# Kernel optimization log

Measured on AMD Instinct MI355X. Metric: run time of the kernel, lower is better.

The kernel has to match this reference:

```python
import jax, jax.numpy as jnp
import numpy as np

LAMB = 1.0
EPS = 1e-16


def setup_inputs() -> dict:
    key = jax.random.key(0)
    kx, km = jax.random.split(key)
    N, D, K = 262144, 128, 64
    x = jax.random.normal(kx, (N, D), dtype=jnp.float32)
    m = jax.random.normal(km, (K, D), dtype=jnp.float32)
    m = m / jnp.linalg.norm(m, axis=1, keepdims=True)  # unit-norm rows like __init__
    return {"x": x, "m": m}


def _entropy(p):
    # replicate torch.where clamping
    p = jnp.where(p <= 0, EPS, p)
    p = jnp.where(p >= 1, 1.0 - EPS, p)
    return -jnp.sum(p * jnp.log(p), axis=-1)


def _p(x, m):
    d2 = (jnp.sum(x * x, axis=-1, keepdims=True)
          - 2.0 * x @ m.T
          + jnp.sum(m * m, axis=-1))  # [N, K]
    return jax.nn.softmax(-d2, axis=-1)


def reference(x, m):
    p = _p(x, m)                      # [N, K]
    intra = jnp.mean(_entropy(p))     # scalar
    mu = jnp.mean(m, axis=0)          # [D]
    p_inter = _p(mu[None, :], m)[0]   # [K]
    inter = _entropy(p_inter)
    total = intra - LAMB * inter
    return (total, intra, inter)
```

## Files before the change

kernel.cpp:

```cpp
#include <hip/hip_runtime.h>
#include <hip/hip_bf16.h>

#define D 128
#define K 64

typedef __attribute__((ext_vector_type(8))) short short8;
typedef __attribute__((ext_vector_type(4))) float f32x4;

__device__ inline short f2bf(float f) {
  union { float f; unsigned u; } v; v.f = f;
  unsigned u = v.u;
  return (short)((u + 0x7fffu + ((u >> 16) & 1u)) >> 16);
}

__global__ void prep_kernel(const float* __restrict__ m, float* ws) {
  int tid = threadIdx.x;
  if (tid < 16) ws[tid] = 0.0f;
  if (tid < K) {
    const float* mr = m + tid * D;
    float s = 0.f;
    for (int d = 0; d < D; ++d) s += mr[d] * mr[d];
    ws[16 + tid] = s;
  }
  short* mb = (short*)(ws + 128);
  for (int i = tid; i < K * D; i += blockDim.x) mb[i] = f2bf(2.0f * m[i]);
}

__launch_bounds__(256)
__global__ void main_kernel(const float* __restrict__ x, float* ws, int nTiles, int totalWaves) {
  const float* mnorm = ws + 16;
  const short* mb = (const short*)(ws + 128);
  const int lane = threadIdx.x & 63;
  const int lid  = lane & 15;
  const int quad = lane >> 4;

  short8 bfr[4][4];
  float mn[4];
#pragma unroll
  for (int jt = 0; jt < 4; ++jt) {
    mn[jt] = mnorm[jt * 16 + lid];
#pragma unroll
    for (int kk = 0; kk < 4; ++kk)
      bfr[jt][kk] = *(const short8*)(mb + (jt * 16 + lid) * D + kk * 32 + quad * 8);
  }

  const int wave = blockIdx.x * (blockDim.x >> 6) + (threadIdx.x >> 6);
  float hacc = 0.f;

  for (int t = wave; t < nTiles; t += totalWaves) {
    const float* xb = x + (size_t)(t * 16 + lid) * D + quad * 8;
    short8 a[4];
#pragma unroll
    for (int kk = 0; kk < 4; ++kk) {
      f32x4 v0 = *(const f32x4*)(xb + kk * 32);
      f32x4 v1 = *(const f32x4*)(xb + kk * 32 + 4);
      short8 av;
      av[0] = f2bf(v0[0]); av[1] = f2bf(v0[1]); av[2] = f2bf(v0[2]); av[3] = f2bf(v0[3]);
      av[4] = f2bf(v1[0]); av[5] = f2bf(v1[1]); av[6] = f2bf(v1[2]); av[7] = f2bf(v1[3]);
      a[kk] = av;
    }

    f32x4 acc[4];
#pragma unroll
    for (int jt = 0; jt < 4; ++jt) acc[jt] = (f32x4){0.f, 0.f, 0.f, 0.f};
#pragma unroll
    for (int kk = 0; kk < 4; ++kk)
#pragma unroll
      for (int jt = 0; jt < 4; ++jt)
        acc[jt] = __builtin_amdgcn_mfma_f32_16x16x32_bf16(a[kk], bfr[jt][kk], acc[jt], 0, 0, 0);

#pragma unroll
    for (int r = 0; r < 4; ++r) {
      float s0 = acc[0][r] - mn[0];
      float s1 = acc[1][r] - mn[1];
      float s2 = acc[2][r] - mn[2];
      float s3 = acc[3][r] - mn[3];
      float mx = fmaxf(fmaxf(s0, s1), fmaxf(s2, s3));
      for (int off = 1; off < 16; off <<= 1) mx = fmaxf(mx, __shfl_xor(mx, off, 64));
      float t0 = s0 - mx, t1 = s1 - mx, t2 = s2 - mx, t3 = s3 - mx;
      float e0 = __expf(t0), e1 = __expf(t1), e2 = __expf(t2), e3 = __expf(t3);
      float S0 = (e0 + e1) + (e2 + e3);
      float S1 = (t0 * e0 + t1 * e1) + (t2 * e2 + t3 * e3);
      for (int off = 1; off < 16; off <<= 1) {
        S0 += __shfl_xor(S0, off, 64);
        S1 += __shfl_xor(S1, off, 64);
      }
      float H = __logf(S0) - S1 / S0;
      if (lid == 0) hacc += H;
    }
  }

  for (int off = 1; off < 64; off <<= 1) hacc += __shfl_xor(hacc, off, 64);
  __shared__ float red[4];
  if (lane == 0) red[threadIdx.x >> 6] = hacc;
  __syncthreads();
  if (threadIdx.x == 0) atomicAdd(ws, red[0] + red[1] + red[2] + red[3]);
}

__global__ void final_kernel(const float* __restrict__ m, const float* ws, float* out, int nRows) {
  __shared__ float mu[D];
  int lane = threadIdx.x;
  for (int d = lane; d < D; d += 64) {
    float s = 0.f;
    for (int j = 0; j < K; ++j) s += m[j * D + d];
    mu[d] = s * (1.0f / K);
  }
  __syncthreads();
  const float* mr = m + lane * D;
  float dot = 0.f;
  for (int d = 0; d < D; ++d) dot += mu[d] * mr[d];
  float s = 2.f * dot - ws[16 + lane];
  float mx = s;
  for (int off = 1; off < 64; off <<= 1) mx = fmaxf(mx, __shfl_xor(mx, off, 64));
  float t = s - mx;
  float e = __expf(t);
  float S0 = e, S1 = t * e;
  for (int off = 1; off < 64; off <<= 1) {
    S0 += __shfl_xor(S0, off, 64);
    S1 += __shfl_xor(S1, off, 64);
  }
  float inter = __logf(S0) - S1 / S0;
  if (lane == 0) {
    float intra = ws[0] / (float)nRows;
    out[0] = intra - inter;
    out[1] = intra;
    out[2] = inter;
  }
}

extern "C" void kernel_launch(void* const* d_in, const int* in_sizes, int n_in,
                              void* d_out, int out_size, void* d_ws, size_t ws_size,
                              hipStream_t stream) {
  const float* x = (const float*)d_in[0];
  const float* m = (const float*)d_in[1];
  float* ws = (float*)d_ws;
  float* out = (float*)d_out;
  const int N = in_sizes[0] / D;
  const int nTiles = N / 16;

  prep_kernel<<<1, 256, 0, stream>>>(m, ws);

  const int blocks = 1024;
  const int totalWaves = blocks * 4;
  main_kernel<<<blocks, 256, 0, stream>>>(x, ws, nTiles, totalWaves);

  final_kernel<<<1, 64, 0, stream>>>(m, ws, out, N);
}
```

Measured before the change: 210.9 us.

## Prefetch next x tile, stage B in swizzled LDS, use DPP row reductions

Loads the next tile's x values into registers before doing the current tile's MFMA and softmax work, so global-load latency is hidden behind compute. The bf16 centroid matrix moves from per-lane registers into XOR-swizzled shared memory, which frees registers; launch bounds are raised to target higher occupancy. The 16-lane max and sum reductions use DPP row rotates instead of shfl_xor (ds_bpermute). The cost is extra LDS reads per MFMA and a block-wide barrier at kernel start.

Measured after the change: 226.2 us. 1.07x slower.

```diff
diff --git a/kernel.cpp b/kernel.cpp
--- a/kernel.cpp
+++ b/kernel.cpp
@@ -1,5 +1,4 @@
 #include <hip/hip_runtime.h>
-#include <hip/hip_bf16.h>
 
 #define D 128
 #define K 64
@@ -11,6 +10,26 @@
   union { float f; unsigned u; } v; v.f = f;
   unsigned u = v.u;
   return (short)((u + 0x7fffu + ((u >> 16) & 1u)) >> 16);
+}
+
+template<int CTRL>
+__device__ inline float dpp_ror(float x) {
+  return __builtin_bit_cast(float, __builtin_amdgcn_update_dpp(
+      0, __builtin_bit_cast(int, x), CTRL, 0xF, 0xF, true));
+}
+__device__ inline float rowsum16(float v) {
+  v += dpp_ror<0x121>(v);
+  v += dpp_ror<0x122>(v);
+  v += dpp_ror<0x124>(v);
+  v += dpp_ror<0x128>(v);
+  return v;
+}
+__device__ inline float rowmax16(float v) {
+  v = fmaxf(v, dpp_ror<0x121>(v));
+  v = fmaxf(v, dpp_ror<0x122>(v));
+  v = fmaxf(v, dpp_ror<0x124>(v));
+  v = fmaxf(v, dpp_ror<0x128>(v));
+  return v;
 }
 
 __global__ void prep_kernel(const float* __restrict__ m, float* ws) {
@@ -26,38 +45,61 @@
   for (int i = tid; i < K * D; i += blockDim.x) mb[i] = f2bf(2.0f * m[i]);
 }
 
-__launch_bounds__(256)
+__launch_bounds__(256, 4)
 __global__ void main_kernel(const float* __restrict__ x, float* ws, int nTiles, int totalWaves) {
+  __shared__ short8 bsm[1024];
   const float* mnorm = ws + 16;
-  const short* mb = (const short*)(ws + 128);
+  const short8* mbv = (const short8*)(ws + 128);
+  for (int i = threadIdx.x; i < 1024; i += blockDim.x)
+    bsm[i ^ ((i >> 4) & 7)] = mbv[i];
+  __syncthreads();
+
   const int lane = threadIdx.x & 63;
   const int lid  = lane & 15;
   const int quad = lane >> 4;
 
-  short8 bfr[4][4];
   float mn[4];
 #pragma unroll
-  for (int jt = 0; jt < 4; ++jt) {
-    mn[jt] = mnorm[jt * 16 + lid];
+  for (int jt = 0; jt < 4; ++jt) mn[jt] = mnorm[jt * 16 + lid];
+
+  int cbase[4];
 #pragma unroll
-    for (int kk = 0; kk < 4; ++kk)
-      bfr[jt][kk] = *(const short8*)(mb + (jt * 16 + lid) * D + kk * 32 + quad * 8);
+  for (int kk = 0; kk < 4; ++kk)
+    cbase[kk] = (lid * 16 + kk * 4 + quad) ^ (lid & 7);
+
+  const int wave = blockIdx.x * (blockDim.x >> 6) + (threadIdx.x >> 6);
+  const size_t laneOff = (size_t)lid * D + quad * 8;
+  float hacc = 0.f;
+
+  f32x4 ld[8];
+  {
+    const float* xb = x + (size_t)wave * (16 * D) + laneOff;
+#pragma unroll
+    for (int kk = 0; kk < 4; ++kk) {
+      ld[2 * kk]     = *(const f32x4*)(xb + kk * 32);
+      ld[2 * kk + 1] = *(const f32x4*)(xb + kk * 32 + 4);
+    }
   }
 
-  const int wave = blockIdx.x * (blockDim.x >> 6) + (threadIdx.x >> 6);
-  float hacc = 0.f;
-
   for (int t = wave; t < nTiles; t += totalWaves) {
-    const float* xb = x + (size_t)(t * 16 + lid) * D + quad * 8;
     short8 a[4];
 #pragma unroll
     for (int kk = 0; kk < 4; ++kk) {
-      f32x4 v0 = *(const f32x4*)(xb + kk * 32);
-      f32x4 v1 = *(const f32x4*)(xb + kk * 32 + 4);
+      f32x4 v0 = ld[2 * kk], v1 = ld[2 * kk + 1];
       short8 av;
       av[0] = f2bf(v0[0]); av[1] = f2bf(v0[1]); av[2] = f2bf(v0[2]); av[3] = f2bf(v0[3]);
       av[4] = f2bf(v1[0]); av[5] = f2bf(v1[1]); av[6] = f2bf(v1[2]); av[7] = f2bf(v1[3]);
       a[kk] = av;
+    }
+
+    int tn = t + totalWaves;
+    if (tn < nTiles) {
+      const float* xb = x + (size_t)tn * (16 * D) + laneOff;
+#pragma unroll
+      for (int kk = 0; kk < 4; ++kk) {
+        ld[2 * kk]     = *(const f32x4*)(xb + kk * 32);
+        ld[2 * kk + 1] = *(const f32x4*)(xb + kk * 32 + 4);
+      }
     }
 
     f32x4 acc[4];
@@ -66,8 +108,10 @@
 #pragma unroll
     for (int kk = 0; kk < 4; ++kk)
 #pragma unroll
-      for (int jt = 0; jt < 4; ++jt)
-        acc[jt] = __builtin_amdgcn_mfma_f32_16x16x32_bf16(a[kk], bfr[jt][kk], acc[jt], 0, 0, 0);
+      for (int jt = 0; jt < 4; ++jt) {
+        short8 b = bsm[cbase[kk] + jt * 256];
+        acc[jt] = __builtin_amdgcn_mfma_f32_16x16x32_bf16(a[kk], b, acc[jt], 0, 0, 0);
+      }
 
 #pragma unroll
     for (int r = 0; r < 4; ++r) {
@@ -75,16 +119,11 @@
       float s1 = acc[1][r] - mn[1];
       float s2 = acc[2][r] - mn[2];
       float s3 = acc[3][r] - mn[3];
-      float mx = fmaxf(fmaxf(s0, s1), fmaxf(s2, s3));
-      for (int off = 1; off < 16; off <<= 1) mx = fmaxf(mx, __shfl_xor(mx, off, 64));
+      float mx = rowmax16(fmaxf(fmaxf(s0, s1), fmaxf(s2, s3)));
       float t0 = s0 - mx, t1 = s1 - mx, t2 = s2 - mx, t3 = s3 - mx;
       float e0 = __expf(t0), e1 = __expf(t1), e2 = __expf(t2), e3 = __expf(t3);
-      float S0 = (e0 + e1) + (e2 + e3);
-      float S1 = (t0 * e0 + t1 * e1) + (t2 * e2 + t3 * e3);
-      for (int off = 1; off < 16; off <<= 1) {
-        S0 += __shfl_xor(S0, off, 64);
-        S1 += __shfl_xor(S1, off, 64);
-      }
+      float S0 = rowsum16((e0 + e1) + (e2 + e3));
+      float S1 = rowsum16((t0 * e0 + t1 * e1) + (t2 * e2 + t3 * e3));
       float H = __logf(S0) - S1 / S0;
       if (lid == 0) hacc += H;
     }
```
